# Kernel tuning notes

Measured on AMD Instinct MI355X. Metric: run time of the kernel, lower is better.

## Reference

```python
import jax, jax.numpy as jnp
import numpy as np

L_LEVELS, N_NODES, MAX_CH, DIM_IN, DIM_OUT = 6, 4096, 8, 256, 256


def reverse_seq(x, length):
    # tf.reverse_sequence: reverse first `length[b]` steps of each row, keep the rest.
    T = x.shape[1]
    t = jnp.arange(T)[None, :]                      # [1,T]
    idx = jnp.where(t < length[:, None], length[:, None] - 1 - t, t)  # [B,T]
    return jnp.take_along_axis(x, idx[:, :, None], axis=1)


def lstm(x, h0, c0, K, R, b):
    # CuDNN/keras gate order i,f,g,o. x: [B,T,D] -> y: [B,T,D]
    def step(carry, xt):
        h, c = carry
        z = xt @ K + h @ R + b
        i, f, g, o = jnp.split(z, 4, axis=-1)
        c = jax.nn.sigmoid(f) * c + jax.nn.sigmoid(i) * jnp.tanh(g)
        h = jax.nn.sigmoid(o) * jnp.tanh(c)
        return (h, c), h
    _, ys = jax.lax.scan(step, (h0, c0), jnp.swapaxes(x, 0, 1))
    return jnp.swapaxes(ys, 0, 1)


def bilstm(x, length, kf, rf, bf, kb, rb, bb, h0f, c0f, h0b, c0b, fc, return_seq):
    B = x.shape[0]
    tile = lambda v: jnp.broadcast_to(v, (B, v.shape[-1]))
    xb = reverse_seq(x, length)
    yf = lstm(x, tile(h0f), tile(c0f), kf, rf, bf)
    yb = lstm(xb, tile(h0b), tile(c0b), kb, rb, bb)
    y = jnp.concatenate([yf, yb], axis=-1)          # [B,T,2D]
    if return_seq:
        return y @ fc                               # NOTE: original does NOT re-reverse yb
    y_last = y[jnp.arange(B), length - 1]           # gather last valid step
    return y_last @ fc


def tree_lstm(tensor, indices, W_kernel, W_bias, kf, rf, bf, kb, rb, bb,
              h0f, c0f, h0b, c0b, fc):
    D = DIM_OUT
    h_tensor = jnp.zeros((1, D), jnp.float32)
    c_tensor = jnp.zeros((1, D), jnp.float32)
    res_h, res_c = [], []
    for lvl in range(L_LEVELS):                     # loop over tree depth (sequential by construction)
        ind = indices[lvl]                          # [N,K]
        x = tensor[lvl]                             # [N,dim_in]
        mask = ind != -1
        maskf = mask.astype(jnp.float32)
        length = mask.sum(axis=1).astype(jnp.int32)
        gidx = jnp.where(mask, ind, 0)
        h = h_tensor[gidx]                          # [N,K,D] irregular gather
        c = c_tensor[gidx]
        Wx = x @ W_kernel + W_bias                  # [N,4D]
        Wf, Wi, Wu, Wo = jnp.split(Wx, 4, axis=-1)

        def gate(g, return_seq):
            return bilstm(h, length, kf[g], rf[g], bf[g], kb[g], rb[g], bb[g],
                          h0f[g], c0f[g], h0b[g], c0b[g], fc[g], return_seq)

        branch_f_k = jax.nn.sigmoid(Wf[:, None, :] + gate(0, True))   # [N,K,D]
        branch_f = jnp.sum(branch_f_k * c * maskf[:, :, None], axis=1)
        branch_i = jax.nn.sigmoid(gate(1, False) + Wi)
        branch_u = jnp.tanh(gate(2, False) + Wu)
        branch_o = jax.nn.sigmoid(gate(3, False) + Wo)
        new_c = branch_i * branch_u + branch_f
        new_h = branch_o * jnp.tanh(new_c)
        res_h.append(new_h)
        res_c.append(new_c)
        h_tensor = jnp.concatenate([jnp.zeros((1, D), jnp.float32), new_h], axis=0)
        c_tensor = jnp.concatenate([jnp.zeros((1, D), jnp.float32), new_c], axis=0)
    return jnp.stack(res_h), jnp.stack(res_c)       # each [L,N,D]


def setup_inputs() -> dict:
    key = jax.random.key(0)
    ks = jax.random.split(key, 16)
    D = DIM_OUT
    s = 0.05
    # tree indices: level 0 = leaves pointing at init row 0; level t>0 indexes 1..N of previous level
    rng = np.random.default_rng(0)
    idx = np.full((L_LEVELS, N_NODES, MAX_CH), -1, np.int32)
    for l in range(L_LEVELS):
        nvalid = rng.integers(1, MAX_CH + 1, size=N_NODES)
        vm = np.arange(MAX_CH)[None, :] < nvalid[:, None]
        if l == 0:
            vals = np.zeros((N_NODES, MAX_CH), np.int32)
        else:
            vals = rng.integers(1, N_NODES + 1, size=(N_NODES, MAX_CH)).astype(np.int32)
        idx[l] = np.where(vm, vals, -1)
    return {
        "tensor": jax.random.normal(ks[0], (L_LEVELS, N_NODES, DIM_IN), jnp.float32),
        "indices": jnp.asarray(idx),
        "W_kernel": jax.random.normal(ks[1], (DIM_IN, 4 * D), jnp.float32) * s,
        "W_bias": jnp.zeros((4 * D,), jnp.float32),
        "lstm_fwd_kernel": jax.random.normal(ks[2], (4, D, 4 * D), jnp.float32) * s,
        "lstm_fwd_rec": jax.random.normal(ks[3], (4, D, 4 * D), jnp.float32) * s,
        "lstm_fwd_bias": jnp.zeros((4, 4 * D), jnp.float32),
        "lstm_bwd_kernel": jax.random.normal(ks[4], (4, D, 4 * D), jnp.float32) * s,
        "lstm_bwd_rec": jax.random.normal(ks[5], (4, D, 4 * D), jnp.float32) * s,
        "lstm_bwd_bias": jnp.zeros((4, 4 * D), jnp.float32),
        "init_fwd_h": jax.random.normal(ks[6], (4, 1, D), jnp.float32) * 0.01,
        "init_fwd_c": jax.random.normal(ks[7], (4, 1, D), jnp.float32) * 0.01,
        "init_bwd_h": jax.random.normal(ks[8], (4, 1, D), jnp.float32) * 0.01,
        "init_bwd_c": jax.random.normal(ks[9], (4, 1, D), jnp.float32) * 0.01,
        "fc_kernel": jax.random.normal(ks[10], (4, 2 * D, D), jnp.float32) * s,
    }


def reference(tensor, indices, W_kernel, W_bias, lstm_fwd_kernel, lstm_fwd_rec,
              lstm_fwd_bias, lstm_bwd_kernel, lstm_bwd_rec, lstm_bwd_bias,
              init_fwd_h, init_fwd_c, init_bwd_h, init_bwd_c, fc_kernel):
    return tree_lstm(tensor, indices, W_kernel, W_bias,
                     lstm_fwd_kernel, lstm_fwd_rec, lstm_fwd_bias,
                     lstm_bwd_kernel, lstm_bwd_rec, lstm_bwd_bias,
                     init_fwd_h, init_fwd_c, init_bwd_h, init_bwd_c, fc_kernel)
```

## Files before the change

kernel.cpp:

```cpp
#include <hip/hip_runtime.h>

typedef unsigned short u16;
typedef float f32x4 __attribute__((ext_vector_type(4)));
typedef __bf16 bf16x8 __attribute__((ext_vector_type(8)));

#define NN   4096
#define NLVL 6
#define LDK  72

static __device__ __forceinline__ u16 f2bf(float f) {
    unsigned int u = __float_as_uint(f);
    u += 0x7fffu + ((u >> 16) & 1u);
    return (u16)(u >> 16);
}
static __device__ __forceinline__ float bf2f(u16 v) {
    return __uint_as_float(((unsigned int)v) << 16);
}
static __device__ __forceinline__ float sigm(float x) { return 1.0f / (1.0f + __expf(-x)); }
static __device__ __forceinline__ float tanh_(float x) { return 2.0f / (1.0f + __expf(-2.0f * x)) - 1.0f; }

__global__ void pack_wcomb(const float* __restrict__ kf, const float* __restrict__ rf,
                           const float* __restrict__ kb, const float* __restrict__ rb,
                           const float* __restrict__ bfw, const float* __restrict__ bbw,
                           u16* __restrict__ WcombT, float* __restrict__ biasP) {
    int C = blockIdx.x, chain = blockIdx.y;
    int g = chain >> 1, dir = chain & 1;
    int ig = C & 3, j = C >> 2;
    int oc = ig * 256 + j;
    const float* Ks = (dir ? kb : kf) + g * (256 * 1024);
    const float* Rs = (dir ? rb : rf) + g * (256 * 1024);
    u16* dst = WcombT + (chain * 1024 + C) * 512;
    for (int it = 0; it < 2; ++it) {
        int k = it * 256 + threadIdx.x;
        float v = (k < 256) ? Ks[k * 1024 + oc] : Rs[(k - 256) * 1024 + oc];
        dst[k] = f2bf(v);
    }
    if (threadIdx.x == 0) biasP[chain * 1024 + C] = (dir ? bbw : bfw)[g * 1024 + oc];
}

__global__ void pack_fcT(const float* __restrict__ fck, u16* __restrict__ fcT) {
    int n = blockIdx.x, g = blockIdx.y;
    u16* dst = fcT + (g * 256 + n) * 512;
    for (int it = 0; it < 2; ++it) {
        int k = it * 256 + threadIdx.x;
        dst[k] = f2bf(fck[(g * 512 + k) * 256 + n]);
    }
}

__global__ void pack_wkT(const float* __restrict__ Wk, u16* __restrict__ WkT) {
    int C = blockIdx.x;
    int k = threadIdx.x;
    WkT[C * 256 + k] = f2bf(Wk[k * 1024 + C]);
}

__global__ void pack_init(const float* __restrict__ ihf, const float* __restrict__ icf,
                          const float* __restrict__ ihb, const float* __restrict__ icb,
                          u16* __restrict__ h0c, float* __restrict__ c0c) {
    int chain = blockIdx.x, j = threadIdx.x;
    int g = chain >> 1, dir = chain & 1;
    h0c[chain * 256 + j] = f2bf((dir ? ihb : ihf)[g * 256 + j]);
    c0c[chain * 256 + j] = (dir ? icb : icf)[g * 256 + j];
}

__global__ void compute_len(const int* __restrict__ indices, int* __restrict__ len_all,
                            int* __restrict__ hist) {
    int lvl = blockIdx.y;
    int b = blockIdx.x * 128 + threadIdx.x;
    const int* ind = indices + ((size_t)lvl * NN + b) * 8;
    int len = 0;
#pragma unroll
    for (int k = 0; k < 8; ++k) len += (ind[k] != -1) ? 1 : 0;
    len_all[lvl * NN + b] = len;
    atomicAdd(&hist[lvl * 8 + (len - 1)], 1);
}

__global__ void build_perm(const int* __restrict__ len_all, const int* __restrict__ hist,
                           int* __restrict__ perm, int* __restrict__ len_p) {
    int lvl = blockIdx.x;
    __shared__ int off[9];
    __shared__ int cur[9];
    if (threadIdx.x == 0) {
        int s = 0;
        for (int L = 8; L >= 1; --L) { off[L] = s; cur[L] = 0; s += hist[lvl * 8 + L - 1]; }
    }
    __syncthreads();
    for (int b = threadIdx.x; b < NN; b += blockDim.x) {
        int len = len_all[lvl * NN + b];
        int pos = off[len] + atomicAdd(&cur[len], 1);
        perm[lvl * NN + pos] = b;
        len_p[lvl * NN + pos] = len;
    }
}

__global__ void convert_x(const float* __restrict__ x, const int* __restrict__ perm,
                          u16* __restrict__ xb) {
    int i = blockIdx.x;
    int orig = perm[i];
    xb[i * 256 + threadIdx.x] = f2bf(x[orig * 256 + threadIdx.x]);
}

__global__ void gather_children(const int* __restrict__ ind, const int* __restrict__ perm,
                                const u16* __restrict__ h_prev, u16* __restrict__ Hc) {
    int i = blockIdx.x;
    int orig = perm[i];
    int k = threadIdx.x >> 5;
    int c0 = (threadIdx.x & 31) * 8;
    int iv = ind[orig * 8 + k];
    uint4 v = make_uint4(0u, 0u, 0u, 0u);
    if (iv >= 1) v = *(const uint4*)(h_prev + (iv - 1) * 256 + c0);
    *(uint4*)(Hc + (i * 8 + k) * 256 + c0) = v;
}

__global__ __launch_bounds__(512)
void lstm_persist(const u16* __restrict__ Hc,
                  const u16* __restrict__ WcombT, const float* __restrict__ biasP,
                  const u16* __restrict__ h0c, const float* __restrict__ c0c,
                  const int* __restrict__ len_p,
                  u16* __restrict__ Y0, u16* __restrict__ ylast) {
    __shared__ u16 hS[64 * 272];
    __shared__ u16 xS[64 * 272];
    __shared__ u16 aS[3][128 * 72];
    const int bid = blockIdx.x;
    const int chain = bid & 7;
    const int bi0 = (bid >> 3) * 64;
    const int dir = chain & 1;
    const int tid = threadIdx.x;
    const int l = tid & 63;
    const int wave = tid >> 6;
    const int wB = wave & 1;
    const int wC = wave >> 1;
    const int crow0 = wC * 32;
    const int bcol0 = wB * 32;
    const int lro = l & 15;
    const int q4 = l >> 4;
    const int kb16 = q4 * 16;

    const u16* Wc = WcombT + (size_t)chain * (1024 * 512);
    char* hSc = (char*)hS;
    char* xSc = (char*)xS;

    const int maxlen = len_p[bi0];

    const int srow = tid >> 3;
    const int sseg = tid & 7;
    const int slen = len_p[bi0 + srow];
    const int wrow = tid >> 2;
    const int wseg = tid & 3;

    {
        const u16* h0 = h0c + chain * 256 + sseg * 32;
#pragma unroll
        for (int i2 = 0; i2 < 4; ++i2) {
            uint4 v = *(const uint4*)(h0 + i2 * 8);
            *(uint4*)(hSc + srow * 544 + sseg * 64 + i2 * 16) = v;
        }
    }
    float c_reg[8][4];
#pragma unroll
    for (int cj = 0; cj < 8; ++cj)
#pragma unroll
        for (int m = 0; m < 2; ++m) {
            int jj = (cj * 128 + crow0 + m * 16 + q4 * 4) >> 2;
            float cv = c0c[chain * 256 + jj];
            c_reg[cj][m * 2 + 0] = cv;
            c_reg[cj][m * 2 + 1] = cv;
        }
    unsigned int hp[8][2];

    const f32x4 zz = {0.f, 0.f, 0.f, 0.f};

    for (int t = 0; t < maxlen; ++t) {
        {
            int ts = dir ? (slen - 1 - t) : t;
            ts = ts < 0 ? 0 : (ts > 7 ? 7 : ts);
            const u16* src = Hc + ((size_t)(bi0 + srow) * 8 + ts) * 256 + sseg * 32;
#pragma unroll
            for (int i2 = 0; i2 < 4; ++i2) {
                uint4 v = *(const uint4*)(src + i2 * 8);
                *(uint4*)(xSc + srow * 544 + sseg * 64 + i2 * 16) = v;
            }
        }
        uint4 pfa[2], pfb[2];
        {
            const u16* s0 = Wc + (size_t)wrow * 512 + wseg * 16;
            uint4 a0 = *(const uint4*)s0, b0 = *(const uint4*)(s0 + 8);
            const u16* s1 = s0 + 64;
            uint4 a1 = *(const uint4*)s1, b1 = *(const uint4*)(s1 + 8);
            const u16* s2 = s0 + 128;
            pfa[0] = *(const uint4*)s2; pfb[0] = *(const uint4*)(s2 + 8);
            char* d0 = (char*)aS[0] + wrow * 144 + wseg * 32;
            *(uint4*)d0 = a0; *(uint4*)(d0 + 16) = b0;
            char* d1 = (char*)aS[1] + wrow * 144 + wseg * 32;
            *(uint4*)d1 = a1; *(uint4*)(d1 + 16) = b1;
        }
        __syncthreads();

        f32x4 acc[2][2];
#pragma unroll
        for (int it = 0; it < 64; ++it) {
            const int cj = it >> 3, kt = it & 7;
            if (kt == 0) { acc[0][0] = zz; acc[0][1] = zz; acc[1][0] = zz; acc[1][1] = zz; }
            if (it + 3 < 64) {
                int nit = it + 3;
                const u16* s = Wc + (size_t)(((nit >> 3) * 128 + wrow) * 512 + (nit & 7) * 64 + wseg * 16);
                pfa[(it + 1) & 1] = *(const uint4*)s;
                pfb[(it + 1) & 1] = *(const uint4*)(s + 8);
            }
            const char* aB = (const char*)aS[it % 3];
            const char* bB = (kt < 4) ? xSc : hSc;
            const int bofs = (kt & 3) * 128;
#pragma unroll
            for (int ks = 0; ks < 2; ++ks) {
                bf16x8 av[2], bv[2];
#pragma unroll
                for (int m = 0; m < 2; ++m) {
                    int r = crow0 + m * 16 + lro;
                    av[m] = *(const bf16x8*)(aB + r * 144 + ks * 64 + kb16);
                }
#pragma unroll
                for (int n = 0; n < 2; ++n) {
                    int r = bcol0 + n * 16 + lro;
                    bv[n] = *(const bf16x8*)(bB + r * 544 + bofs + ks * 64 + kb16);
                }
#pragma unroll
                for (int m = 0; m < 2; ++m)
#pragma unroll
                    for (int n = 0; n < 2; ++n)
                        acc[m][n] = __builtin_amdgcn_mfma_f32_16x16x32_bf16(av[m], bv[n], acc[m][n], 0, 0, 0);
            }
            if (kt == 7) {
#pragma unroll
                for (int m = 0; m < 2; ++m) {
                    int Crow = cj * 128 + crow0 + m * 16 + q4 * 4;
                    float4 bias = *(const float4*)(biasP + chain * 1024 + Crow);
                    unsigned int packed = 0;
#pragma unroll
                    for (int n = 0; n < 2; ++n) {
                        float zi = acc[m][n][0] + bias.x;
                        float zf = acc[m][n][1] + bias.y;
                        float zg = acc[m][n][2] + bias.z;
                        float zo = acc[m][n][3] + bias.w;
                        float cn = sigm(zf) * c_reg[cj][m * 2 + n] + sigm(zi) * tanh_(zg);
                        float hn = sigm(zo) * tanh_(cn);
                        c_reg[cj][m * 2 + n] = cn;
                        packed |= ((unsigned int)f2bf(hn)) << (16 * n);
                    }
                    hp[cj][m] = packed;
                }
            }
            __syncthreads();
            if (it + 2 < 64) {
                char* d = (char*)aS[(it + 2) % 3] + wrow * 144 + wseg * 32;
                *(uint4*)d = pfa[it & 1];
                *(uint4*)(d + 16) = pfb[it & 1];
            }
        }
#pragma unroll
        for (int cj = 0; cj < 8; ++cj)
#pragma unroll
            for (int m = 0; m < 2; ++m) {
                int jj = (cj * 128 + crow0 + m * 16 + q4 * 4) >> 2;
#pragma unroll
                for (int n = 0; n < 2; ++n) {
                    int bl = bcol0 + n * 16 + lro;
                    hS[bl * 272 + jj] = (u16)((hp[cj][m] >> (16 * n)) & 0xffffu);
                }
            }
        __syncthreads();
        if (chain < 2) {
            u16* dst = Y0 + (size_t)((bi0 + srow) * 8 + t) * 512 + dir * 256 + sseg * 32;
#pragma unroll
            for (int i2 = 0; i2 < 4; ++i2)
                *(uint4*)(dst + i2 * 8) = *(const uint4*)(hSc + srow * 544 + sseg * 64 + i2 * 16);
        } else if (t == slen - 1) {
            u16* dst = ylast + (size_t)((chain >> 1) - 1) * (NN * 512)
                     + (size_t)(bi0 + srow) * 512 + dir * 256 + sseg * 32;
#pragma unroll
            for (int i2 = 0; i2 < 4; ++i2)
                *(uint4*)(dst + i2 * 8) = *(const uint4*)(hSc + srow * 544 + sseg * 64 + i2 * 16);
        }
    }
}

__global__ __launch_bounds__(256)
void gemm_bf16(const u16* __restrict__ A, long long sAz,
               const u16* __restrict__ BT, long long sBz,
               void* __restrict__ Craw, long long sCz,
               const float* __restrict__ bias, int K, int obf) {
    __shared__ u16 As[128 * LDK];
    __shared__ u16 Bs[128 * LDK];
    const int z = blockIdx.z;
    A += z * sAz; BT += z * sBz;
    const int N = gridDim.y * 128;
    const int bm0 = blockIdx.x * 128;
    const int bn0 = blockIdx.y * 128;
    const int tid = threadIdx.x;
    const int l = tid & 63;
    const int wave = tid >> 6;
    const int wrow = (wave >> 1) * 64;
    const int wcol = (wave & 1) * 64;

    const u16* srcA[4]; const u16* srcB[4]; u16* dstA[4]; u16* dstB[4];
#pragma unroll
    for (int i = 0; i < 4; ++i) {
        int idx = i * 256 + tid;
        int row = idx >> 3;
        int kE = (idx & 7) * 8;
        srcA[i] = A + (long long)(bm0 + row) * K + kE;
        srcB[i] = BT + (long long)(bn0 + row) * K + kE;
        dstA[i] = As + row * LDK + kE;
        dstB[i] = Bs + row * LDK + kE;
    }
    f32x4 acc[4][4];
    const f32x4 zz = {0.f, 0.f, 0.f, 0.f};
#pragma unroll
    for (int m = 0; m < 4; ++m)
#pragma unroll
        for (int n = 0; n < 4; ++n) acc[m][n] = zz;

    for (int kk = 0; kk < K; kk += 64) {
#pragma unroll
        for (int i = 0; i < 4; ++i) {
            *(uint4*)dstA[i] = *(const uint4*)(srcA[i] + kk);
            *(uint4*)dstB[i] = *(const uint4*)(srcB[i] + kk);
        }
        __syncthreads();
        const int lro = l & 15;
        const int lk = (l >> 4) * 8;
#pragma unroll
        for (int k2 = 0; k2 < 64; k2 += 32) {
            bf16x8 av[4], bv[4];
#pragma unroll
            for (int m = 0; m < 4; ++m)
                av[m] = *(const bf16x8*)(As + (wrow + m * 16 + lro) * LDK + k2 + lk);
#pragma unroll
            for (int n = 0; n < 4; ++n)
                bv[n] = *(const bf16x8*)(Bs + (wcol + n * 16 + lro) * LDK + k2 + lk);
#pragma unroll
            for (int m = 0; m < 4; ++m)
#pragma unroll
                for (int n = 0; n < 4; ++n)
                    acc[m][n] = __builtin_amdgcn_mfma_f32_16x16x32_bf16(av[m], bv[n], acc[m][n], 0, 0, 0);
        }
        __syncthreads();
    }
#pragma unroll
    for (int m = 0; m < 4; ++m)
#pragma unroll
        for (int n = 0; n < 4; ++n) {
            int Cg = bn0 + wcol + n * 16 + (l & 15);
            float bv = bias ? bias[Cg] : 0.f;
#pragma unroll
            for (int r = 0; r < 4; ++r) {
                int R = bm0 + wrow + m * 16 + (l >> 4) * 4 + r;
                float v = acc[m][n][r] + bv;
                if (obf) ((u16*)Craw)[z * sCz + (long long)R * N + Cg] = f2bf(v);
                else     ((float*)Craw)[z * sCz + (long long)R * N + Cg] = v;
            }
        }
}

__global__ void combine_level(const u16* __restrict__ G0, const u16* __restrict__ G13,
                              const u16* __restrict__ Wx, const int* __restrict__ ind,
                              const int* __restrict__ perm, const float* __restrict__ cprev,
                              float* __restrict__ outH, float* __restrict__ outC,
                              u16* __restrict__ hnext, float* __restrict__ cnext) {
    int i = blockIdx.x;
    int orig = perm[i];
    int j = threadIdx.x;
    float wf = bf2f(Wx[i * 1024 + j]);
    float wi = bf2f(Wx[i * 1024 + 256 + j]);
    float wu = bf2f(Wx[i * 1024 + 512 + j]);
    float wo = bf2f(Wx[i * 1024 + 768 + j]);
    float bfa = 0.f;
#pragma unroll
    for (int k = 0; k < 8; ++k) {
        int iv = ind[orig * 8 + k];
        if (iv == -1) continue;
        float cc = (iv >= 1) ? cprev[(iv - 1) * 256 + j] : 0.f;
        bfa += sigm(wf + bf2f(G0[(i * 8 + k) * 256 + j])) * cc;
    }
    float bi = sigm(bf2f(G13[0 * NN * 256 + i * 256 + j]) + wi);
    float bu = tanh_(bf2f(G13[1 * NN * 256 + i * 256 + j]) + wu);
    float bo = sigm(bf2f(G13[2 * NN * 256 + i * 256 + j]) + wo);
    float nc = bi * bu + bfa;
    float nh = bo * tanh_(nc);
    outH[orig * 256 + j] = nh;
    outC[orig * 256 + j] = nc;
    hnext[orig * 256 + j] = f2bf(nh);
    cnext[orig * 256 + j] = nc;
}

extern "C" void kernel_launch(void* const* d_in, const int* in_sizes, int n_in,
                              void* d_out, int out_size, void* d_ws, size_t ws_size,
                              hipStream_t stream) {
    (void)in_sizes; (void)n_in; (void)out_size; (void)ws_size;
    const float* tensor  = (const float*)d_in[0];
    const int*   indices = (const int*)d_in[1];
    const float* Wk      = (const float*)d_in[2];
    const float* Wb      = (const float*)d_in[3];
    const float* kf      = (const float*)d_in[4];
    const float* rf      = (const float*)d_in[5];
    const float* bfw     = (const float*)d_in[6];
    const float* kb      = (const float*)d_in[7];
    const float* rb      = (const float*)d_in[8];
    const float* bbw     = (const float*)d_in[9];
    const float* ihf     = (const float*)d_in[10];
    const float* icf     = (const float*)d_in[11];
    const float* ihb     = (const float*)d_in[12];
    const float* icb     = (const float*)d_in[13];
    const float* fck     = (const float*)d_in[14];
    float* out = (float*)d_out;

    char* p = (char*)d_ws;
    auto take = [&](size_t bytes) -> char* {
        char* r = p;
        p += (bytes + 255) & ~(size_t)255;
        return r;
    };
    u16*   WcombT    = (u16*)  take(8ull * 1024 * 512 * 2);
    float* biasP     = (float*)take(8ull * 1024 * 4);
    u16*   WkT       = (u16*)  take(1024ull * 256 * 2);
    u16*   fcT       = (u16*)  take(4ull * 256 * 512 * 2);
    u16*   h0c       = (u16*)  take(8ull * 256 * 2);
    float* c0c       = (float*)take(8ull * 256 * 4);
    int*   perm      = (int*)  take((size_t)NLVL * NN * 4);
    int*   len_all   = (int*)  take((size_t)NLVL * NN * 4);
    int*   len_p     = (int*)  take((size_t)NLVL * NN * 4);
    int*   hist      = (int*)  take((size_t)NLVL * 8 * 4);
    u16*   Xbf       = (u16*)  take((size_t)NN * 256 * 2);
    u16*   Hc        = (u16*)  take((size_t)NN * 8 * 256 * 2);
    u16*   Y0        = (u16*)  take((size_t)NN * 8 * 512 * 2);
    u16*   ylast     = (u16*)  take(3ull * NN * 512 * 2);
    u16*   Wx        = (u16*)  take((size_t)NN * 1024 * 2);
    u16*   G0        = (u16*)  take((size_t)NN * 8 * 256 * 2);
    u16*   G13       = (u16*)  take(3ull * NN * 256 * 2);
    u16*   hprev[2]  = { (u16*)take((size_t)NN * 256 * 2), (u16*)take((size_t)NN * 256 * 2) };
    float* cprev[2]  = { (float*)take((size_t)NN * 256 * 4), (float*)take((size_t)NN * 256 * 4) };

    hipMemsetAsync(hist, 0, (size_t)NLVL * 8 * 4, stream);
    pack_wcomb<<<dim3(1024, 8), 256, 0, stream>>>(kf, rf, kb, rb, bfw, bbw, WcombT, biasP);
    pack_fcT<<<dim3(256, 4), 256, 0, stream>>>(fck, fcT);
    pack_wkT<<<dim3(1024), 256, 0, stream>>>(Wk, WkT);
    pack_init<<<dim3(8), 256, 0, stream>>>(ihf, icf, ihb, icb, h0c, c0c);
    compute_len<<<dim3(32, NLVL), 128, 0, stream>>>(indices, len_all, hist);
    build_perm<<<dim3(NLVL), 256, 0, stream>>>(len_all, hist, perm, len_p);

    for (int lvl = 0; lvl < NLVL; ++lvl) {
        const int* ind = indices + (size_t)lvl * NN * 8;
        const int* permL = perm + (size_t)lvl * NN;
        const int* lenpL = len_p + (size_t)lvl * NN;
        int cur = lvl & 1, nxt = cur ^ 1;

        convert_x<<<dim3(NN), 256, 0, stream>>>(tensor + (size_t)lvl * NN * 256, permL, Xbf);
        gather_children<<<dim3(NN), 256, 0, stream>>>(ind, permL, hprev[cur], Hc);

        gemm_bf16<<<dim3(32, 8, 1), 256, 0, stream>>>(Xbf, 0, WkT, 0, Wx, 0, Wb, 256, 1);

        lstm_persist<<<dim3(512), 512, 0, stream>>>(Hc, WcombT, biasP, h0c, c0c, lenpL, Y0, ylast);

        gemm_bf16<<<dim3(256, 2, 1), 256, 0, stream>>>(Y0, 0, fcT, 0, G0, 0, nullptr, 512, 1);
        gemm_bf16<<<dim3(32, 2, 3), 256, 0, stream>>>(
            ylast, (long long)NN * 512, fcT + 256 * 512, (long long)256 * 512,
            G13, (long long)NN * 256, nullptr, 512, 1);

        combine_level<<<dim3(NN), 256, 0, stream>>>(
            G0, G13, Wx, ind, permL, cprev[cur],
            out + (size_t)lvl * NN * 256,
            out + (size_t)NLVL * NN * 256 + (size_t)lvl * NN * 256,
            hprev[nxt], cprev[nxt]);
    }
}
```

Measured before the change: 3.612 ms.

## Load LSTM weights directly from MFMA-fragment-packed global layout, drop LDS staging

The recurrent weight matrix is repacked so that each 16-row, 32-k tile is contiguous and matches the MFMA A-fragment layout. Each wave now reads its A fragments straight from global/L2 with a register double-buffer, instead of staging them through a triple-buffered LDS ring that needed a barrier every k-step. Each wave covers 128 gate rows across the full batch tile in two halves, and the per-step barriers drop from 64 to a few. LDS use shrinks and launch_bounds asks for 2 blocks per CU, which lets more waves hide latency. In exchange every weight fetch goes through global/L2 for each step, and the accumulator tile and register pressure grow.

After: 6.242 ms. 72.8% more time.

```diff
diff --git a/kernel.cpp b/kernel.cpp
--- a/kernel.cpp
+++ b/kernel.cpp
@@ -22,18 +22,20 @@
 __global__ void pack_wcomb(const float* __restrict__ kf, const float* __restrict__ rf,
                            const float* __restrict__ kb, const float* __restrict__ rb,
                            const float* __restrict__ bfw, const float* __restrict__ bbw,
-                           u16* __restrict__ WcombT, float* __restrict__ biasP) {
+                           u16* __restrict__ W2, float* __restrict__ biasP) {
     int C = blockIdx.x, chain = blockIdx.y;
     int g = chain >> 1, dir = chain & 1;
     int ig = C & 3, j = C >> 2;
     int oc = ig * 256 + j;
+    int ct = C >> 4, lro = C & 15;
     const float* Ks = (dir ? kb : kf) + g * (256 * 1024);
     const float* Rs = (dir ? rb : rf) + g * (256 * 1024);
-    u16* dst = WcombT + (chain * 1024 + C) * 512;
+    u16* base = W2 + (size_t)chain * (1024 * 512);
     for (int it = 0; it < 2; ++it) {
         int k = it * 256 + threadIdx.x;
         float v = (k < 256) ? Ks[k * 1024 + oc] : Rs[(k - 256) * 1024 + oc];
-        dst[k] = f2bf(v);
+        int ks = k >> 5, kk = k & 31;
+        base[(size_t)(ct * 16 + ks) * 512 + lro * 32 + kk] = f2bf(v);
     }
     if (threadIdx.x == 0) biasP[chain * 1024 + C] = (dir ? bbw : bfw)[g * 1024 + oc];
 }
@@ -111,15 +113,14 @@
     *(uint4*)(Hc + (i * 8 + k) * 256 + c0) = v;
 }
 
-__global__ __launch_bounds__(512)
+__global__ __launch_bounds__(512, 2)
 void lstm_persist(const u16* __restrict__ Hc,
-                  const u16* __restrict__ WcombT, const float* __restrict__ biasP,
+                  const u16* __restrict__ W2, const float* __restrict__ biasP,
                   const u16* __restrict__ h0c, const float* __restrict__ c0c,
                   const int* __restrict__ len_p,
                   u16* __restrict__ Y0, u16* __restrict__ ylast) {
-    __shared__ u16 hS[64 * 272];
-    __shared__ u16 xS[64 * 272];
-    __shared__ u16 aS[3][128 * 72];
+    __shared__ u16 xS[64 * 264];
+    __shared__ u16 hS[64 * 264];
     const int bid = blockIdx.x;
     const int chain = bid & 7;
     const int bi0 = (bid >> 3) * 64;
@@ -127,44 +128,31 @@
     const int tid = threadIdx.x;
     const int l = tid & 63;
     const int wave = tid >> 6;
-    const int wB = wave & 1;
-    const int wC = wave >> 1;
-    const int crow0 = wC * 32;
-    const int bcol0 = wB * 32;
     const int lro = l & 15;
     const int q4 = l >> 4;
-    const int kb16 = q4 * 16;
-
-    const u16* Wc = WcombT + (size_t)chain * (1024 * 512);
-    char* hSc = (char*)hS;
-    char* xSc = (char*)xS;
 
     const int maxlen = len_p[bi0];
-
     const int srow = tid >> 3;
     const int sseg = tid & 7;
     const int slen = len_p[bi0 + srow];
-    const int wrow = tid >> 2;
-    const int wseg = tid & 3;
+
+    const u16* Wf = W2 + (size_t)chain * (1024 * 512);
+    char* xSc = (char*)xS;
+    char* hSc = (char*)hS;
 
     {
         const u16* h0 = h0c + chain * 256 + sseg * 32;
 #pragma unroll
-        for (int i2 = 0; i2 < 4; ++i2) {
-            uint4 v = *(const uint4*)(h0 + i2 * 8);
-            *(uint4*)(hSc + srow * 544 + sseg * 64 + i2 * 16) = v;
-        }
+        for (int i2 = 0; i2 < 4; ++i2)
+            *(uint4*)(hSc + srow * 528 + sseg * 64 + i2 * 16) = *(const uint4*)(h0 + i2 * 8);
     }
     float c_reg[8][4];
 #pragma unroll
-    for (int cj = 0; cj < 8; ++cj)
-#pragma unroll
-        for (int m = 0; m < 2; ++m) {
-            int jj = (cj * 128 + crow0 + m * 16 + q4 * 4) >> 2;
-            float cv = c0c[chain * 256 + jj];
-            c_reg[cj][m * 2 + 0] = cv;
-            c_reg[cj][m * 2 + 1] = cv;
-        }
+    for (int hm = 0; hm < 8; ++hm) {
+        float cv = c0c[chain * 256 + wave * 32 + hm * 4 + q4];
+#pragma unroll
+        for (int n = 0; n < 4; ++n) c_reg[hm][n] = cv;
+    }
     unsigned int hp[8][2];
 
     const f32x4 zz = {0.f, 0.f, 0.f, 0.f};
@@ -172,112 +160,98 @@
     for (int t = 0; t < maxlen; ++t) {
         {
             int ts = dir ? (slen - 1 - t) : t;
-            ts = ts < 0 ? 0 : (ts > 7 ? 7 : ts);
+            ts = ts < 0 ? 0 : ts;
             const u16* src = Hc + ((size_t)(bi0 + srow) * 8 + ts) * 256 + sseg * 32;
 #pragma unroll
-            for (int i2 = 0; i2 < 4; ++i2) {
-                uint4 v = *(const uint4*)(src + i2 * 8);
-                *(uint4*)(xSc + srow * 544 + sseg * 64 + i2 * 16) = v;
+            for (int i2 = 0; i2 < 4; ++i2)
+                *(uint4*)(xSc + srow * 528 + sseg * 64 + i2 * 16) = *(const uint4*)(src + i2 * 8);
+        }
+        __syncthreads();
+
+#pragma unroll
+        for (int half = 0; half < 2; ++half) {
+            f32x4 acc[4][4];
+#pragma unroll
+            for (int m = 0; m < 4; ++m)
+#pragma unroll
+                for (int n = 0; n < 4; ++n) acc[m][n] = zz;
+
+            const int lfo = lro * 32 + q4 * 8;
+            bf16x8 avp[2][4];
+#pragma unroll
+            for (int m = 0; m < 4; ++m)
+                avp[0][m] = *(const bf16x8*)(Wf + (size_t)((wave * 8 + half * 4 + m) * 16) * 512 + lfo);
+#pragma unroll
+            for (int ks = 0; ks < 16; ++ks) {
+                if (ks < 15) {
+#pragma unroll
+                    for (int m = 0; m < 4; ++m)
+                        avp[(ks + 1) & 1][m] =
+                            *(const bf16x8*)(Wf + (size_t)((wave * 8 + half * 4 + m) * 16 + ks + 1) * 512 + lfo);
+                }
+                const char* bB = (ks < 8) ? xSc : hSc;
+                const int bofs = (ks & 7) * 64 + q4 * 16;
+                bf16x8 bv[4];
+#pragma unroll
+                for (int n = 0; n < 4; ++n)
+                    bv[n] = *(const bf16x8*)(bB + (n * 16 + lro) * 528 + bofs);
+#pragma unroll
+                for (int m = 0; m < 4; ++m)
+#pragma unroll
+                    for (int n = 0; n < 4; ++n)
+                        acc[m][n] = __builtin_amdgcn_mfma_f32_16x16x32_bf16(avp[ks & 1][m], bv[n], acc[m][n], 0, 0, 0);
             }
-        }
-        uint4 pfa[2], pfb[2];
-        {
-            const u16* s0 = Wc + (size_t)wrow * 512 + wseg * 16;
-            uint4 a0 = *(const uint4*)s0, b0 = *(const uint4*)(s0 + 8);
-            const u16* s1 = s0 + 64;
-            uint4 a1 = *(const uint4*)s1, b1 = *(const uint4*)(s1 + 8);
-            const u16* s2 = s0 + 128;
-            pfa[0] = *(const uint4*)s2; pfb[0] = *(const uint4*)(s2 + 8);
-            char* d0 = (char*)aS[0] + wrow * 144 + wseg * 32;
-            *(uint4*)d0 = a0; *(uint4*)(d0 + 16) = b0;
-            char* d1 = (char*)aS[1] + wrow * 144 + wseg * 32;
-            *(uint4*)d1 = a1; *(uint4*)(d1 + 16) = b1;
+#pragma unroll
+            for (int m = 0; m < 4; ++m) {
+                int hm = half * 4 + m;
+                int Crow = (wave * 8 + hm) * 16 + q4 * 4;
+                float4 bias = *(const float4*)(biasP + chain * 1024 + Crow);
+                unsigned int p0 = 0, p1 = 0;
+#pragma unroll
+                for (int n = 0; n < 4; ++n) {
+                    float zi = acc[m][n][0] + bias.x;
+                    float zf = acc[m][n][1] + bias.y;
+                    float zg = acc[m][n][2] + bias.z;
+                    float zo = acc[m][n][3] + bias.w;
+                    float cn = sigm(zf) * c_reg[hm][n] + sigm(zi) * tanh_(zg);
+                    float hn = sigm(zo) * tanh_(cn);
+                    c_reg[hm][n] = cn;
+                    unsigned int hb = (unsigned int)f2bf(hn);
+                    if (n < 2) p0 |= hb << (16 * n);
+                    else       p1 |= hb << (16 * (n - 2));
+                }
+                hp[hm][0] = p0;
+                hp[hm][1] = p1;
+            }
         }
         __syncthreads();
 
-        f32x4 acc[2][2];
-#pragma unroll
-        for (int it = 0; it < 64; ++it) {
-            const int cj = it >> 3, kt = it & 7;
-            if (kt == 0) { acc[0][0] = zz; acc[0][1] = zz; acc[1][0] = zz; acc[1][1] = zz; }
-            if (it + 3 < 64) {
-                int nit = it + 3;
-                const u16* s = Wc + (size_t)(((nit >> 3) * 128 + wrow) * 512 + (nit & 7) * 64 + wseg * 16);
-                pfa[(it + 1) & 1] = *(const uint4*)s;
-                pfb[(it + 1) & 1] = *(const uint4*)(s + 8);
-            }
-            const char* aB = (const char*)aS[it % 3];
-            const char* bB = (kt < 4) ? xSc : hSc;
-            const int bofs = (kt & 3) * 128;
-#pragma unroll
-            for (int ks = 0; ks < 2; ++ks) {
-                bf16x8 av[2], bv[2];
-#pragma unroll
-                for (int m = 0; m < 2; ++m) {
-                    int r = crow0 + m * 16 + lro;
-                    av[m] = *(const bf16x8*)(aB + r * 144 + ks * 64 + kb16);
-                }
-#pragma unroll
-                for (int n = 0; n < 2; ++n) {
-                    int r = bcol0 + n * 16 + lro;
-                    bv[n] = *(const bf16x8*)(bB + r * 544 + bofs + ks * 64 + kb16);
-                }
-#pragma unroll
-                for (int m = 0; m < 2; ++m)
-#pragma unroll
-                    for (int n = 0; n < 2; ++n)
-                        acc[m][n] = __builtin_amdgcn_mfma_f32_16x16x32_bf16(av[m], bv[n], acc[m][n], 0, 0, 0);
-            }
-            if (kt == 7) {
-#pragma unroll
-                for (int m = 0; m < 2; ++m) {
-                    int Crow = cj * 128 + crow0 + m * 16 + q4 * 4;
-                    float4 bias = *(const float4*)(biasP + chain * 1024 + Crow);
-                    unsigned int packed = 0;
-#pragma unroll
-                    for (int n = 0; n < 2; ++n) {
-                        float zi = acc[m][n][0] + bias.x;
-                        float zf = acc[m][n][1] + bias.y;
-                        float zg = acc[m][n][2] + bias.z;
-                        float zo = acc[m][n][3] + bias.w;
-                        float cn = sigm(zf) * c_reg[cj][m * 2 + n] + sigm(zi) * tanh_(zg);
-                        float hn = sigm(zo) * tanh_(cn);
-                        c_reg[cj][m * 2 + n] = cn;
-                        packed |= ((unsigned int)f2bf(hn)) << (16 * n);
-                    }
-                    hp[cj][m] = packed;
+#pragma unroll
+        for (int hm = 0; hm < 8; ++hm) {
+            int jj = wave * 32 + hm * 4 + q4;
+#pragma unroll
+            for (int n = 0; n < 4; ++n) {
+                unsigned int val = (hp[hm][n >> 1] >> (16 * (n & 1))) & 0xffffu;
+                unsigned int part = (unsigned int)__shfl_xor((int)val, 16);
+                if ((q4 & 1) == 0) {
+                    int col = n * 16 + lro;
+                    *(unsigned int*)(hSc + col * 528 + jj * 2) = val | (part << 16);
                 }
             }
-            __syncthreads();
-            if (it + 2 < 64) {
-                char* d = (char*)aS[(it + 2) % 3] + wrow * 144 + wseg * 32;
-                *(uint4*)d = pfa[it & 1];
-                *(uint4*)(d + 16) = pfb[it & 1];
-            }
-        }
-#pragma unroll
-        for (int cj = 0; cj < 8; ++cj)
-#pragma unroll
-            for (int m = 0; m < 2; ++m) {
-                int jj = (cj * 128 + crow0 + m * 16 + q4 * 4) >> 2;
-#pragma unroll
-                for (int n = 0; n < 2; ++n) {
-                    int bl = bcol0 + n * 16 + lro;
-                    hS[bl * 272 + jj] = (u16)((hp[cj][m] >> (16 * n)) & 0xffffu);
-                }
-            }
+        }
         __syncthreads();
+
         if (chain < 2) {
-            u16* dst = Y0 + (size_t)((bi0 + srow) * 8 + t) * 512 + dir * 256 + sseg * 32;
+            u16* dst = Y0 + ((size_t)(bi0 + srow) * 8 + t) * 512 + dir * 256 + sseg * 32;
 #pragma unroll
             for (int i2 = 0; i2 < 4; ++i2)
-                *(uint4*)(dst + i2 * 8) = *(const uint4*)(hSc + srow * 544 + sseg * 64 + i2 * 16);
+                *(uint4*)(dst + i2 * 8) = *(const uint4*)(hSc + srow * 528 + sseg * 64 + i2 * 16);
         } else if (t == slen - 1) {
             u16* dst = ylast + (size_t)((chain >> 1) - 1) * (NN * 512)
                      + (size_t)(bi0 + srow) * 512 + dir * 256 + sseg * 32;
 #pragma unroll
             for (int i2 = 0; i2 < 4; ++i2)
-                *(uint4*)(dst + i2 * 8) = *(const uint4*)(hSc + srow * 544 + sseg * 64 + i2 * 16);
+                *(uint4*)(dst + i2 * 8) = *(const uint4*)(hSc + srow * 528 + sseg * 64 + i2 * 16);
         }
     }
 }
@@ -418,7 +392,7 @@
         p += (bytes + 255) & ~(size_t)255;
         return r;
     };
-    u16*   WcombT    = (u16*)  take(8ull * 1024 * 512 * 2);
+    u16*   W2        = (u16*)  take(8ull * 1024 * 512 * 2);
     float* biasP     = (float*)take(8ull * 1024 * 4);
     u16*   WkT       = (u16*)  take(1024ull * 256 * 2);
     u16*   fcT       = (u16*)  take(4ull * 256 * 512 * 2);
@@ -439,7 +413,7 @@
     float* cprev[2]  = { (float*)take((size_t)NN * 256 * 4), (float*)take((size_t)NN * 256 * 4) };
 
     hipMemsetAsync(hist, 0, (size_t)NLVL * 8 * 4, stream);
-    pack_wcomb<<<dim3(1024, 8), 256, 0, stream>>>(kf, rf, kb, rb, bfw, bbw, WcombT, biasP);
+    pack_wcomb<<<dim3(1024, 8), 256, 0, stream>>>(kf, rf, kb, rb, bfw, bbw, W2, biasP);
     pack_fcT<<<dim3(256, 4), 256, 0, stream>>>(fck, fcT);
     pack_wkT<<<dim3(1024), 256, 0, stream>>>(Wk, WkT);
     pack_init<<<dim3(8), 256, 0, stream>>>(ihf, icf, ihb, icb, h0c, c0c);
@@ -457,7 +431,7 @@
 
         gemm_bf16<<<dim3(32, 8, 1), 256, 0, stream>>>(Xbf, 0, WkT, 0, Wx, 0, Wb, 256, 1);
 
-        lstm_persist<<<dim3(512), 512, 0, stream>>>(Hc, WcombT, biasP, h0c, c0c, lenpL, Y0, ylast);
+        lstm_persist<<<dim3(512), 512, 0, stream>>>(Hc, W2, biasP, h0c, c0c, lenpL, Y0, ylast);
 
         gemm_bf16<<<dim3(256, 2, 1), 256, 0, stream>>>(Y0, 0, fcT, 0, G0, 0, nullptr, 512, 1);
         gemm_bf16<<<dim3(32, 2, 3), 256, 0, stream>>>(
```
